# Performance work log

Measured on AMD Instinct MI355X. Metric: run time of the kernel, lower is better.

## Reference

```python
import jax, jax.numpy as jnp
import numpy as np

B = 4096
NUM_FEATURES = 2048
NUM_NEURONS = 1024
NUM_TARGETS = 8
NNZ1 = 65536
NNZ2 = 8192


def _sparse_linear(x, w, b, rows, cols, n_out):
    """y[b, o] = sum_{e: rows[e]==o} w[e] * x[b, cols[e]] + b[o].

    x: [B, n_in], w: [nnz], rows/cols: [nnz] int, b: [n_out].
    """
    prod = x[:, cols] * w  # [B, nnz] gather + elementwise
    # segment_sum reduces over leading axis -> work on [nnz, B]
    y = jax.ops.segment_sum(prod.T, rows, num_segments=n_out)  # [n_out, B]
    return y.T + b


def setup_inputs() -> dict:
    key = jax.random.key(0)
    ks = jax.random.split(key, 9)
    x = jax.random.normal(ks[0], (B, NUM_FEATURES), dtype=jnp.float32)
    w1 = jax.random.normal(ks[1], (NNZ1,), dtype=jnp.float32) * 0.05
    b1 = jax.random.normal(ks[2], (NUM_NEURONS,), dtype=jnp.float32) * 0.05
    w2 = jax.random.normal(ks[3], (NNZ2,), dtype=jnp.float32) * 0.05
    b2 = jax.random.normal(ks[4], (NUM_TARGETS,), dtype=jnp.float32) * 0.05
    conn1_out = jax.random.randint(ks[5], (NNZ1,), 0, NUM_NEURONS, dtype=jnp.int64 if jax.config.jax_enable_x64 else jnp.int32)
    conn1_in = jax.random.randint(ks[6], (NNZ1,), 0, NUM_FEATURES, dtype=conn1_out.dtype)
    conn2_out = jax.random.randint(ks[7], (NNZ2,), 0, NUM_TARGETS, dtype=conn1_out.dtype)
    conn2_in = jax.random.randint(ks[8], (NNZ2,), 0, NUM_NEURONS, dtype=conn1_out.dtype)
    return {
        "x": x, "w1": w1, "b1": b1, "w2": w2, "b2": b2,
        "conn1_out": conn1_out, "conn1_in": conn1_in,
        "conn2_out": conn2_out, "conn2_in": conn2_in,
    }


def reference(x, w1, b1, w2, b2, conn1_out, conn1_in, conn2_out, conn2_in):
    h = jax.nn.sigmoid(_sparse_linear(x, w1, b1, conn1_out, conn1_in, b1.shape[0]))
    out = _sparse_linear(h, w2, b2, conn2_out, conn2_in, b2.shape[0])
    # num_targets = 8 != 1, so no final sigmoid (matches CrossEntropyLoss path)
    return out
```

## Files before the change

### kernel.cpp

```cpp
#include <hip/hip_runtime.h>
#include <math.h>

#define BATCH 4096
#define NFEAT 2048
#define NNEUR 1024
#define NTGT  8
#define NNZ1  65536
#define NNZ2  8192

#define BM 128
#define BN 64
#define BK 64
#define KSTEPS (NFEAT / BK)

typedef short  bf16x8 __attribute__((ext_vector_type(8)));
typedef float  f32x4  __attribute__((ext_vector_type(4)));

#define OFF_W1F  ((size_t)0)
#define OFF_W2D  ((size_t)8388608)
#define OFF_W1B  ((size_t)8421376)
#define OFF_XB   ((size_t)12615680)
#define OFF_PART ((size_t)29392896)

#define ZERO_FLOAT4 526336

__device__ __forceinline__ unsigned short f2bf(float f) {
    union { float f; unsigned int u; } a; a.f = f;
    unsigned int u = a.u;
    u += 0x7fffu + ((u >> 16) & 1u);
    return (unsigned short)(u >> 16);
}

__global__ void k_zero4(float4* __restrict__ p) {
    int i = blockIdx.x * blockDim.x + threadIdx.x;
    p[i] = make_float4(0.f, 0.f, 0.f, 0.f);
}

__global__ void k_build(const float* __restrict__ w1, const int* __restrict__ c1o,
                        const int* __restrict__ c1i,
                        const float* __restrict__ w2, const int* __restrict__ c2o,
                        const int* __restrict__ c2i,
                        float* __restrict__ W1f, float* __restrict__ W2d) {
    int i = blockIdx.x * blockDim.x + threadIdx.x;
    if (i < NNZ1) {
        atomicAdd(&W1f[(size_t)c1o[i] * NFEAT + c1i[i]], w1[i]);
    } else {
        int j = i - NNZ1;
        if (j < NNZ2) atomicAdd(&W2d[c2i[j] * NTGT + c2o[j]], w2[j]);
    }
}

__global__ void k_convert(const float* __restrict__ W1f, const float* __restrict__ x,
                          unsigned short* __restrict__ W1b, unsigned short* __restrict__ xb) {
    int i = blockIdx.x * blockDim.x + threadIdx.x;
    const int nW = NNEUR * NFEAT / 4;
    const int nX = BATCH * NFEAT / 4;
    if (i < nW) {
        float4 v = ((const float4*)W1f)[i];
        ushort4 o;
        o.x = f2bf(v.x); o.y = f2bf(v.y); o.z = f2bf(v.z); o.w = f2bf(v.w);
        ((ushort4*)W1b)[i] = o;
    } else if (i < nW + nX) {
        int j = i - nW;
        float4 v = ((const float4*)x)[j];
        ushort4 o;
        o.x = f2bf(v.x); o.y = f2bf(v.y); o.z = f2bf(v.z); o.w = f2bf(v.w);
        ((ushort4*)xb)[j] = o;
    }
}

__global__ __launch_bounds__(256) void k_gemm(const unsigned short* __restrict__ W1b,
                                              const unsigned short* __restrict__ xb,
                                              const float* __restrict__ b1,
                                              const float* __restrict__ W2d,
                                              float* __restrict__ partial) {
    __shared__ unsigned short ldsA[2][BM * BK];
    __shared__ unsigned short ldsB[2][BN * BK];
    __shared__ float s_w2[BM][NTGT];
    __shared__ float s_b1[BM];
    __shared__ float s_pt[2][BN][NTGT];

    int bid = blockIdx.x;
    int v   = bid >> 3;
    int n0  = ((bid & 7) * 8 + (v >> 3)) * BN;
    int mt  = v & 7;
    int m0  = mt * BM;

    int tid  = threadIdx.x;
    int wv   = tid >> 6;
    int lane = tid & 63;
    int wm = wv >> 1, wn = wv & 1;
    int lr = lane & 15, lg = lane >> 4;

    for (int i = tid; i < BM * NTGT; i += 256)
        s_w2[i >> 3][i & 7] = W2d[(m0 + (i >> 3)) * NTGT + (i & 7)];
    if (tid < BM) s_b1[tid] = b1[m0 + tid];

    f32x4 zero4 = {0.f, 0.f, 0.f, 0.f};
    f32x4 acc[4][2];
#pragma unroll
    for (int i = 0; i < 4; ++i)
#pragma unroll
        for (int j = 0; j < 2; ++j) acc[i][j] = zero4;

    const unsigned short* gAp[4]; int iwA[4];
#pragma unroll
    for (int c = 0; c < 4; ++c) {
        int u = c * 256 + tid, row = u >> 3, s = u & 7;
        gAp[c] = &W1b[(size_t)(m0 + row) * NFEAT + s * 8];
        iwA[c] = row * 8 + (s ^ (row & 7));
    }
    const unsigned short* gBp[2]; int iwB[2];
#pragma unroll
    for (int c = 0; c < 2; ++c) {
        int u = c * 256 + tid, row = u >> 3, s = u & 7;
        gBp[c] = &xb[(size_t)(n0 + row) * NFEAT + s * 8];
        iwB[c] = row * 8 + (s ^ (row & 7));
    }

    bf16x8 ra0, ra1, ra2, ra3, rb0, rb1;

#define LOADR(T) do { int kk = (T) * BK;                            \
        ra0 = *(const bf16x8*)(gAp[0] + kk);                        \
        ra1 = *(const bf16x8*)(gAp[1] + kk);                        \
        ra2 = *(const bf16x8*)(gAp[2] + kk);                        \
        ra3 = *(const bf16x8*)(gAp[3] + kk);                        \
        rb0 = *(const bf16x8*)(gBp[0] + kk);                        \
        rb1 = *(const bf16x8*)(gBp[1] + kk); } while (0)

#define STORE(BUF) do {                                             \
        bf16x8* dA = (bf16x8*)&ldsA[BUF][0];                        \
        bf16x8* dB = (bf16x8*)&ldsB[BUF][0];                        \
        dA[iwA[0]] = ra0; dA[iwA[1]] = ra1;                         \
        dA[iwA[2]] = ra2; dA[iwA[3]] = ra3;                         \
        dB[iwB[0]] = rb0; dB[iwB[1]] = rb1; } while (0)

    bf16x8 af0[4], af1[4], bg0[2], bg1[2];

#define READF(BUF) do {                                             \
        const unsigned short* bA = ldsA[BUF];                       \
        const unsigned short* bB = ldsB[BUF];                       \
        _Pragma("unroll")                                           \
        for (int i = 0; i < 4; ++i) {                               \
            int rowa = wm * 64 + i * 16 + lr;                       \
            af0[i] = *(const bf16x8*)&bA[(rowa * 8 + ((lg)     ^ (rowa & 7))) * 8]; \
            af1[i] = *(const bf16x8*)&bA[(rowa * 8 + ((4 + lg) ^ (rowa & 7))) * 8]; \
        }                                                           \
        _Pragma("unroll")                                           \
        for (int j = 0; j < 2; ++j) {                               \
            int rowb = wn * 32 + j * 16 + lr;                       \
            bg0[j] = *(const bf16x8*)&bB[(rowb * 8 + ((lg)     ^ (rowb & 7))) * 8]; \
            bg1[j] = *(const bf16x8*)&bB[(rowb * 8 + ((4 + lg) ^ (rowb & 7))) * 8]; \
        }                                                           \
    } while (0)

#define MFMAS() do {                                                \
        _Pragma("unroll")                                           \
        for (int i = 0; i < 4; ++i)                                 \
            _Pragma("unroll")                                       \
            for (int j = 0; j < 2; ++j)                             \
                acc[i][j] = __builtin_amdgcn_mfma_f32_16x16x32_bf16(af0[i], bg0[j], acc[i][j], 0, 0, 0); \
        _Pragma("unroll")                                           \
        for (int i = 0; i < 4; ++i)                                 \
            _Pragma("unroll")                                       \
            for (int j = 0; j < 2; ++j)                             \
                acc[i][j] = __builtin_amdgcn_mfma_f32_16x16x32_bf16(af1[i], bg1[j], acc[i][j], 0, 0, 0); \
    } while (0)

    LOADR(0);
    asm volatile("s_waitcnt vmcnt(0)" ::: "memory");
    STORE(0);
    LOADR(1);
    asm volatile("s_waitcnt lgkmcnt(0)" ::: "memory");
    __builtin_amdgcn_s_barrier();

    for (int t = 0; t < KSTEPS; ++t) {
        if (t + 1 < KSTEPS) {
            asm volatile("s_waitcnt vmcnt(0)" ::: "memory");
            __builtin_amdgcn_sched_barrier(0);
            STORE((t + 1) & 1);
            if (t + 2 < KSTEPS) LOADR(t + 2);
            __builtin_amdgcn_sched_barrier(0);
        }
        READF(t & 1);
        asm volatile("s_waitcnt lgkmcnt(0)" ::: "memory");
        __builtin_amdgcn_sched_barrier(0);
        __builtin_amdgcn_s_setprio(1);
        MFMAS();
        __builtin_amdgcn_s_setprio(0);
        __builtin_amdgcn_sched_barrier(0);
        __builtin_amdgcn_s_barrier();
    }

#undef LOADR
#undef STORE
#undef READF
#undef MFMAS

    float pt[2][NTGT];
#pragma unroll
    for (int j = 0; j < 2; ++j)
#pragma unroll
        for (int t = 0; t < NTGT; ++t) pt[j][t] = 0.f;

#pragma unroll
    for (int i = 0; i < 4; ++i) {
#pragma unroll
        for (int r = 0; r < 4; ++r) {
            int ml = wm * 64 + i * 16 + lg * 4 + r;
            float bn = s_b1[ml];
#pragma unroll
            for (int j = 0; j < 2; ++j) {
                float h = 1.f / (1.f + __expf(-(acc[i][j][r] + bn)));
#pragma unroll
                for (int t = 0; t < NTGT; ++t)
                    pt[j][t] += h * s_w2[ml][t];
            }
        }
    }
#pragma unroll
    for (int j = 0; j < 2; ++j)
#pragma unroll
        for (int t = 0; t < NTGT; ++t) {
            float val = pt[j][t];
            val += __shfl_xor(val, 16, 64);
            val += __shfl_xor(val, 32, 64);
            pt[j][t] = val;
        }
    if (lg == 0) {
#pragma unroll
        for (int j = 0; j < 2; ++j) {
            int nl = wn * 32 + j * 16 + lr;
#pragma unroll
            for (int t = 0; t < NTGT; ++t)
                s_pt[wm][nl][t] = pt[j][t];
        }
    }
    __syncthreads();
    for (int idx = tid; idx < BN * NTGT; idx += 256) {
        int nl = idx >> 3, t = idx & 7;
        partial[((size_t)mt * BATCH + (n0 + nl)) * NTGT + t] = s_pt[0][nl][t] + s_pt[1][nl][t];
    }
}

__global__ void k_reduce(const float* __restrict__ partial, const float* __restrict__ b2,
                         float* __restrict__ out) {
    int i = blockIdx.x * blockDim.x + threadIdx.x;
    float v = b2[i & 7];
#pragma unroll
    for (int c = 0; c < 8; ++c) v += partial[(size_t)c * BATCH * NTGT + i];
    out[i] = v;
}

extern "C" void kernel_launch(void* const* d_in, const int* in_sizes, int n_in,
                              void* d_out, int out_size, void* d_ws, size_t ws_size,
                              hipStream_t stream) {
    (void)in_sizes; (void)n_in; (void)out_size; (void)ws_size;
    const float* x   = (const float*)d_in[0];
    const float* w1  = (const float*)d_in[1];
    const float* b1  = (const float*)d_in[2];
    const float* w2  = (const float*)d_in[3];
    const float* b2  = (const float*)d_in[4];
    const int*   c1o = (const int*)d_in[5];
    const int*   c1i = (const int*)d_in[6];
    const int*   c2o = (const int*)d_in[7];
    const int*   c2i = (const int*)d_in[8];
    float* out = (float*)d_out;

    char* ws = (char*)d_ws;
    float*          W1f  = (float*)(ws + OFF_W1F);
    float*          W2d  = (float*)(ws + OFF_W2D);
    unsigned short* W1b  = (unsigned short*)(ws + OFF_W1B);
    unsigned short* xb   = (unsigned short*)(ws + OFF_XB);
    float*          part = (float*)(ws + OFF_PART);

    k_zero4<<<ZERO_FLOAT4 / 256, 256, 0, stream>>>((float4*)ws);

    k_build<<<(NNZ1 + NNZ2) / 256, 256, 0, stream>>>(w1, c1o, c1i, w2, c2o, c2i, W1f, W2d);

    k_convert<<<(NNEUR * NFEAT / 4 + BATCH * NFEAT / 4) / 256, 256, 0, stream>>>(W1f, x, W1b, xb);

    k_gemm<<<(NNEUR / BM) * (BATCH / BN), 256, 0, stream>>>(W1b, xb, b1, W2d, part);

    k_reduce<<<BATCH * NTGT / 256, 256, 0, stream>>>(part, b2, out);
}
```

Baseline: 55.60 us.

## Fuse x bf16 conversion into GEMM loads and deepen prefetch pipeline

```diff
diff --git a/kernel.cpp b/kernel.cpp
--- a/kernel.cpp
+++ b/kernel.cpp
@@ -19,7 +19,6 @@
 #define OFF_W1F  ((size_t)0)
 #define OFF_W2D  ((size_t)8388608)
 #define OFF_W1B  ((size_t)8421376)
-#define OFF_XB   ((size_t)12615680)
 #define OFF_PART ((size_t)29392896)
 
 #define ZERO_FLOAT4 526336
@@ -29,6 +28,15 @@
     unsigned int u = a.u;
     u += 0x7fffu + ((u >> 16) & 1u);
     return (unsigned short)(u >> 16);
+}
+
+__device__ __forceinline__ uint4 pk8(float4 lo, float4 hi) {
+    uint4 r;
+    asm("v_cvt_pk_bf16_f32 %0, %1, %2" : "=v"(r.x) : "v"(lo.x), "v"(lo.y));
+    asm("v_cvt_pk_bf16_f32 %0, %1, %2" : "=v"(r.y) : "v"(lo.z), "v"(lo.w));
+    asm("v_cvt_pk_bf16_f32 %0, %1, %2" : "=v"(r.z) : "v"(hi.x), "v"(hi.y));
+    asm("v_cvt_pk_bf16_f32 %0, %1, %2" : "=v"(r.w) : "v"(hi.z), "v"(hi.w));
+    return r;
 }
 
 __global__ void k_zero4(float4* __restrict__ p) {
@@ -50,27 +58,16 @@
     }
 }
 
-__global__ void k_convert(const float* __restrict__ W1f, const float* __restrict__ x,
-                          unsigned short* __restrict__ W1b, unsigned short* __restrict__ xb) {
+__global__ void k_convert(const float* __restrict__ W1f, unsigned short* __restrict__ W1b) {
     int i = blockIdx.x * blockDim.x + threadIdx.x;
-    const int nW = NNEUR * NFEAT / 4;
-    const int nX = BATCH * NFEAT / 4;
-    if (i < nW) {
-        float4 v = ((const float4*)W1f)[i];
-        ushort4 o;
-        o.x = f2bf(v.x); o.y = f2bf(v.y); o.z = f2bf(v.z); o.w = f2bf(v.w);
-        ((ushort4*)W1b)[i] = o;
-    } else if (i < nW + nX) {
-        int j = i - nW;
-        float4 v = ((const float4*)x)[j];
-        ushort4 o;
-        o.x = f2bf(v.x); o.y = f2bf(v.y); o.z = f2bf(v.z); o.w = f2bf(v.w);
-        ((ushort4*)xb)[j] = o;
-    }
+    float4 v = ((const float4*)W1f)[i];
+    ushort4 o;
+    o.x = f2bf(v.x); o.y = f2bf(v.y); o.z = f2bf(v.z); o.w = f2bf(v.w);
+    ((ushort4*)W1b)[i] = o;
 }
 
 __global__ __launch_bounds__(256) void k_gemm(const unsigned short* __restrict__ W1b,
-                                              const unsigned short* __restrict__ xb,
+                                              const float* __restrict__ x,
                                               const float* __restrict__ b1,
                                               const float* __restrict__ W2d,
                                               float* __restrict__ partial) {
@@ -95,6 +92,8 @@
     for (int i = tid; i < BM * NTGT; i += 256)
         s_w2[i >> 3][i & 7] = W2d[(m0 + (i >> 3)) * NTGT + (i & 7)];
     if (tid < BM) s_b1[tid] = b1[m0 + tid];
+    asm volatile("s_waitcnt vmcnt(0) lgkmcnt(0)" ::: "memory");
+    __builtin_amdgcn_sched_barrier(0);
 
     f32x4 zero4 = {0.f, 0.f, 0.f, 0.f};
     f32x4 acc[4][2];
@@ -103,39 +102,41 @@
 #pragma unroll
         for (int j = 0; j < 2; ++j) acc[i][j] = zero4;
 
-    const unsigned short* gAp[4]; int iwA[4];
-#pragma unroll
-    for (int c = 0; c < 4; ++c) {
-        int u = c * 256 + tid, row = u >> 3, s = u & 7;
-        gAp[c] = &W1b[(size_t)(m0 + row) * NFEAT + s * 8];
-        iwA[c] = row * 8 + (s ^ (row & 7));
-    }
-    const unsigned short* gBp[2]; int iwB[2];
-#pragma unroll
-    for (int c = 0; c < 2; ++c) {
-        int u = c * 256 + tid, row = u >> 3, s = u & 7;
-        gBp[c] = &xb[(size_t)(n0 + row) * NFEAT + s * 8];
-        iwB[c] = row * 8 + (s ^ (row & 7));
-    }
-
-    bf16x8 ra0, ra1, ra2, ra3, rb0, rb1;
-
-#define LOADR(T) do { int kk = (T) * BK;                            \
-        ra0 = *(const bf16x8*)(gAp[0] + kk);                        \
-        ra1 = *(const bf16x8*)(gAp[1] + kk);                        \
-        ra2 = *(const bf16x8*)(gAp[2] + kk);                        \
-        ra3 = *(const bf16x8*)(gAp[3] + kk);                        \
-        rb0 = *(const bf16x8*)(gBp[0] + kk);                        \
-        rb1 = *(const bf16x8*)(gBp[1] + kk); } while (0)
-
-#define STORE(BUF) do {                                             \
+    int r0 = tid >> 3, s0 = tid & 7;
+    const unsigned short* gA0 = &W1b[(size_t)(m0 + r0) * NFEAT + s0 * 8];
+    const unsigned short* gA1 = gA0 + 32 * NFEAT;
+    const unsigned short* gA2 = gA0 + 64 * NFEAT;
+    const unsigned short* gA3 = gA0 + 96 * NFEAT;
+    const float* gB0 = &x[(size_t)(n0 + r0) * NFEAT + s0 * 8];
+    const float* gB1 = gB0 + 32 * NFEAT;
+    const int iw0 = r0 * 8 + (s0 ^ (r0 & 7));
+    const int iw1 = iw0 + 256, iw2 = iw0 + 512, iw3 = iw0 + 768;
+
+    bf16x8 A0a, A0b, A0c, A0d;  float4 B0a, B0b, B0c, B0d;
+    bf16x8 A1a, A1b, A1c, A1d;  float4 B1a, B1b, B1c, B1d;
+    bf16x8 af0[4], af1[4], bg0[2], bg1[2];
+
+#define LOADS0(T) do { int kk = (T) * BK;                           \
+        A0a = *(const bf16x8*)(gA0 + kk); A0b = *(const bf16x8*)(gA1 + kk); \
+        A0c = *(const bf16x8*)(gA2 + kk); A0d = *(const bf16x8*)(gA3 + kk); \
+        B0a = *(const float4*)(gB0 + kk); B0b = *(const float4*)(gB0 + kk + 4); \
+        B0c = *(const float4*)(gB1 + kk); B0d = *(const float4*)(gB1 + kk + 4); } while (0)
+#define LOADS1(T) do { int kk = (T) * BK;                           \
+        A1a = *(const bf16x8*)(gA0 + kk); A1b = *(const bf16x8*)(gA1 + kk); \
+        A1c = *(const bf16x8*)(gA2 + kk); A1d = *(const bf16x8*)(gA3 + kk); \
+        B1a = *(const float4*)(gB0 + kk); B1b = *(const float4*)(gB0 + kk + 4); \
+        B1c = *(const float4*)(gB1 + kk); B1d = *(const float4*)(gB1 + kk + 4); } while (0)
+
+#define STORE0(BUF) do {                                            \
         bf16x8* dA = (bf16x8*)&ldsA[BUF][0];                        \
-        bf16x8* dB = (bf16x8*)&ldsB[BUF][0];                        \
-        dA[iwA[0]] = ra0; dA[iwA[1]] = ra1;                         \
-        dA[iwA[2]] = ra2; dA[iwA[3]] = ra3;                         \
-        dB[iwB[0]] = rb0; dB[iwB[1]] = rb1; } while (0)
-
-    bf16x8 af0[4], af1[4], bg0[2], bg1[2];
+        dA[iw0] = A0a; dA[iw1] = A0b; dA[iw2] = A0c; dA[iw3] = A0d; \
+        uint4* dB = (uint4*)&ldsB[BUF][0];                          \
+        dB[iw0] = pk8(B0a, B0b); dB[iw1] = pk8(B0c, B0d); } while (0)
+#define STORE1(BUF) do {                                            \
+        bf16x8* dA = (bf16x8*)&ldsA[BUF][0];                        \
+        dA[iw0] = A1a; dA[iw1] = A1b; dA[iw2] = A1c; dA[iw3] = A1d; \
+        uint4* dB = (uint4*)&ldsB[BUF][0];                          \
+        dB[iw0] = pk8(B1a, B1b); dB[iw1] = pk8(B1c, B1d); } while (0)
 
 #define READF(BUF) do {                                             \
         const unsigned short* bA = ldsA[BUF];                       \
@@ -167,35 +168,62 @@
                 acc[i][j] = __builtin_amdgcn_mfma_f32_16x16x32_bf16(af1[i], bg1[j], acc[i][j], 0, 0, 0); \
     } while (0)
 
-    LOADR(0);
-    asm volatile("s_waitcnt vmcnt(0)" ::: "memory");
-    STORE(0);
-    LOADR(1);
-    asm volatile("s_waitcnt lgkmcnt(0)" ::: "memory");
+#define WAIT_VM(N)  asm volatile("s_waitcnt vmcnt(" #N ")" ::: "memory"); \
+                    __builtin_amdgcn_sched_barrier(0)
+#define WAIT_LGKM() asm volatile("s_waitcnt lgkmcnt(0)" ::: "memory");    \
+                    __builtin_amdgcn_sched_barrier(0)
+
+    LOADS0(0);
+    LOADS1(1);
+    WAIT_VM(8);
+    STORE0(0);
+    WAIT_LGKM();
     __builtin_amdgcn_s_barrier();
 
-    for (int t = 0; t < KSTEPS; ++t) {
-        if (t + 1 < KSTEPS) {
-            asm volatile("s_waitcnt vmcnt(0)" ::: "memory");
-            __builtin_amdgcn_sched_barrier(0);
-            STORE((t + 1) & 1);
-            if (t + 2 < KSTEPS) LOADR(t + 2);
-            __builtin_amdgcn_sched_barrier(0);
-        }
-        READF(t & 1);
-        asm volatile("s_waitcnt lgkmcnt(0)" ::: "memory");
+#pragma unroll 1
+    for (int t = 0; t < KSTEPS - 2; t += 2) {
+        LOADS0(t + 2);
         __builtin_amdgcn_sched_barrier(0);
-        __builtin_amdgcn_s_setprio(1);
-        MFMAS();
-        __builtin_amdgcn_s_setprio(0);
+        READF(0);
+        WAIT_LGKM();
+        __builtin_amdgcn_s_setprio(1); MFMAS(); __builtin_amdgcn_s_setprio(0);
         __builtin_amdgcn_sched_barrier(0);
+        WAIT_VM(8);
+        STORE1(1);
+        WAIT_LGKM();
         __builtin_amdgcn_s_barrier();
-    }
-
-#undef LOADR
-#undef STORE
+        LOADS1(t + 3);
+        __builtin_amdgcn_sched_barrier(0);
+        READF(1);
+        WAIT_LGKM();
+        __builtin_amdgcn_s_setprio(1); MFMAS(); __builtin_amdgcn_s_setprio(0);
+        __builtin_amdgcn_sched_barrier(0);
+        WAIT_VM(8);
+        STORE0(0);
+        WAIT_LGKM();
+        __builtin_amdgcn_s_barrier();
+    }
+    READF(0);
+    WAIT_LGKM();
+    __builtin_amdgcn_s_setprio(1); MFMAS(); __builtin_amdgcn_s_setprio(0);
+    __builtin_amdgcn_sched_barrier(0);
+    WAIT_VM(0);
+    STORE1(1);
+    WAIT_LGKM();
+    __builtin_amdgcn_s_barrier();
+    READF(1);
+    WAIT_LGKM();
+    __builtin_amdgcn_s_setprio(1); MFMAS(); __builtin_amdgcn_s_setprio(0);
+    __builtin_amdgcn_sched_barrier(0);
+
+#undef LOADS0
+#undef LOADS1
+#undef STORE0
+#undef STORE1
 #undef READF
 #undef MFMAS
+#undef WAIT_VM
+#undef WAIT_LGKM
 
     float pt[2][NTGT];
 #pragma unroll
@@ -271,16 +299,15 @@
     float*          W1f  = (float*)(ws + OFF_W1F);
     float*          W2d  = (float*)(ws + OFF_W2D);
     unsigned short* W1b  = (unsigned short*)(ws + OFF_W1B);
-    unsigned short* xb   = (unsigned short*)(ws + OFF_XB);
     float*          part = (float*)(ws + OFF_PART);
 
     k_zero4<<<ZERO_FLOAT4 / 256, 256, 0, stream>>>((float4*)ws);
 
     k_build<<<(NNZ1 + NNZ2) / 256, 256, 0, stream>>>(w1, c1o, c1i, w2, c2o, c2i, W1f, W2d);
 
-    k_convert<<<(NNEUR * NFEAT / 4 + BATCH * NFEAT / 4) / 256, 256, 0, stream>>>(W1f, x, W1b, xb);
-
-    k_gemm<<<(NNEUR / BM) * (BATCH / BN), 256, 0, stream>>>(W1b, xb, b1, W2d, part);
+    k_convert<<<NNEUR * NFEAT / 4 / 256, 256, 0, stream>>>(W1f, W1b);
+
+    k_gemm<<<(NNEUR / BM) * (BATCH / BN), 256, 0, stream>>>(W1b, x, b1, W2d, part);
 
     k_reduce<<<BATCH * NTGT / 256, 256, 0, stream>>>(part, b2, out);
 }
```

Measured after the change: 53.33 us. 4.1% less time.
